# Performance work log

Hardware: AMD Instinct MI355X
Metric: run time of the kernel (lower is better)

The kernel has to match this reference:

```python
import math
import jax, jax.numpy as jnp
import numpy as np

D = 4  # BWGNN d


def calculate_theta2(d):
    # Faithful numeric reimplementation of the sympy version.
    # f_i(x) = (x/2)^i (1-x/2)^(d-i) / (2*Beta(i+1, d+1-i)); the original code
    # keeps only the d lowest-order (ascending) coefficients, dropping x^d.
    thetas = []
    for i in range(d):
        c1 = np.zeros(i + 1); c1[i] = 0.5 ** i                      # (x/2)^i
        c2 = np.array([math.comb(d - i, j) * (-0.5) ** j
                       for j in range(d - i + 1)])                   # (1-x/2)^(d-i)
        c = np.convolve(c1, c2)                                      # ascending, len d+1
        B = math.factorial(i) * math.factorial(d - i) / math.factorial(d + 1)
        c = c / (2.0 * B)
        thetas.append([float(c[j]) for j in range(d)])               # coeff[d-i] slicing
    return thetas

THETAS = calculate_theta2(D)


def setup_inputs() -> dict:
    key = jax.random.key(0)
    k1, k2, k3, k4 = jax.random.split(key, 4)
    N, E, F_in, H = 100000, 1600000, 128, 64
    feature = jax.random.normal(k1, (N, F_in), dtype=jnp.float32)
    edge_index = jax.random.randint(k2, (2, E), 0, N, dtype=jnp.int32)
    W = jax.random.normal(k3, (F_in, H), dtype=jnp.float32) * 0.05
    b = jax.random.normal(k4, (H,), dtype=jnp.float32) * 0.05
    return {"feature": feature, "edge_index": edge_index, "W": W, "b": b}


def reference(feature, edge_index, W, b):
    N = feature.shape[0]
    src, dst = edge_index[0], edge_index[1]
    # out_degrees: number of out-edges per node (src side), clamped to >= 1
    deg = jax.ops.segment_sum(jnp.ones_like(src, dtype=jnp.float32), src,
                              num_segments=N)
    D_invsqrt = jnp.maximum(deg, 1.0) ** -0.5  # [N]
    D_invsqrt = D_invsqrt[:, None]             # [N,1]

    h = jax.nn.leaky_relu(feature @ W + b, negative_slope=0.01)  # [N,H]

    def unn_laplacian(feat):
        # feat - D^{-1/2} A^T D^{-1/2} feat  (copy_u + sum over dst)
        msg = (feat * D_invsqrt)[src]                          # [E,H]
        agg = jax.ops.segment_sum(msg, dst, num_segments=N)    # [N,H]
        return feat - agg * D_invsqrt

    outs = []
    for theta in THETAS:
        feat = h
        acc = theta[0] * feat
        for k in range(1, len(theta)):
            feat = unn_laplacian(feat)
            acc = acc + theta[k] * feat
        outs.append(acc)
    return jnp.concatenate(outs, axis=1)  # [N, len(THETAS)*H]
```

## Files before the change

### kernel.cpp

```cpp
#include <hip/hip_runtime.h>

#define THREADS 256
#define T1 4096
#define BCAP 8192
#define NBMAX 512

__device__ __forceinline__ float bf2f(unsigned short u) {
    return __uint_as_float(((unsigned int)u) << 16);
}
__device__ __forceinline__ unsigned short f2bf(float x) {
    unsigned int u = __float_as_uint(x);
    u += 0x7fffu + ((u >> 16) & 1u);
    return (unsigned short)(u >> 16);
}
__device__ __forceinline__ float blo(unsigned int x) { return __uint_as_float(x << 16); }
__device__ __forceinline__ float bhi(unsigned int x) { return __uint_as_float(x & 0xffff0000u); }

__global__ void zero_kernel(int* __restrict__ p, int n) {
    const int i = blockIdx.x * blockDim.x + threadIdx.x;
    if (i < n) p[i] = 0;
}

__global__ void bin_kernel(const int* __restrict__ src, const int* __restrict__ dst,
                           int* __restrict__ gFillD, unsigned int* __restrict__ gBufD,
                           int* __restrict__ gFillS, unsigned int* __restrict__ gBufS,
                           int E, int tiles) {
    __shared__ int cnt[NBMAX], scanB[NBMAX], gbase[NBMAX], place[NBMAX];
    __shared__ unsigned int stage[T1], addr[T1];
    const int tid = threadIdx.x;
    const bool isS = blockIdx.x >= tiles;
    const int tile = isS ? blockIdx.x - tiles : blockIdx.x;
    const int* key = isS ? src : dst;
    int* gFill = isS ? gFillS : gFillD;
    unsigned int* gBuf = isS ? gBufS : gBufD;
    const int tileStart = tile * T1;
    const int tileCnt = min(T1, E - tileStart);

    for (int i = tid; i < NBMAX; i += THREADS) { cnt[i] = 0; place[i] = 0; }
    __syncthreads();

    for (int i = tid; i < tileCnt; i += THREADS)
        atomicAdd(&cnt[key[tileStart + i] >> 8], 1);
    __syncthreads();

    if (tid < 64) {
        const int base = tid * 8;
        int loc[8]; int s = 0;
        #pragma unroll
        for (int k = 0; k < 8; ++k) { loc[k] = s; s += cnt[base + k]; }
        int run = s;
        #pragma unroll
        for (int off = 1; off < 64; off <<= 1) {
            int t = __shfl_up(run, off);
            if (tid >= off) run += t;
        }
        const int excl = run - s;
        #pragma unroll
        for (int k = 0; k < 8; ++k) scanB[base + k] = excl + loc[k];
    }
    __syncthreads();

    for (int i = tid; i < NBMAX; i += THREADS)
        gbase[i] = atomicAdd(&gFill[i], cnt[i]);
    __syncthreads();

    for (int i = tid; i < tileCnt; i += THREADS) {
        const int kk = key[tileStart + i];
        const int b = kk >> 8;
        const unsigned int rec = isS ? (unsigned int)(kk & 255)
                                     : (((unsigned int)(kk & 255) << 17) | (unsigned int)src[tileStart + i]);
        const int pos = atomicAdd(&place[b], 1);
        const int li = scanB[b] + pos;
        const int gi = gbase[b] + pos;
        stage[li] = rec;
        addr[li] = (gi < BCAP) ? (unsigned int)(b * BCAP + gi) : 0xFFFFFFFFu;
    }
    __syncthreads();

    for (int i = tid; i < tileCnt; i += THREADS) {
        const unsigned int a = addr[i];
        if (a != 0xFFFFFFFFu) gBuf[a] = stage[i];
    }
}

__global__ void scanb_kernel(const int* __restrict__ gFill, int* __restrict__ gBase,
                             int* __restrict__ rowptr, int nb, int N) {
    __shared__ int s[NBMAX];
    const int tid = threadIdx.x;
    const int v = (tid < nb) ? min(gFill[tid], BCAP) : 0;
    s[tid] = v;
    __syncthreads();
    for (int off = 1; off < NBMAX; off <<= 1) {
        int t = (tid >= off) ? s[tid - off] : 0;
        __syncthreads();
        s[tid] += t;
        __syncthreads();
    }
    if (tid < nb) gBase[tid] = s[tid] - v;
    if (tid == NBMAX - 1) rowptr[N] = s[NBMAX - 1];
}

__global__ void csr_kernel(const int* __restrict__ gFillD, const int* __restrict__ gBase,
                           const unsigned int* __restrict__ gBufD,
                           const int* __restrict__ gFillS, const unsigned int* __restrict__ gBufS,
                           int* __restrict__ rowptr, int* __restrict__ col,
                           int* __restrict__ deg, int N) {
    __shared__ int fillT[256], offT[256], place[256], sc[256];
    __shared__ int colT[BCAP];
    __shared__ int nwrite;
    const int tid = threadIdx.x;
    const int b = blockIdx.x;
    const int nrec = min(gFillD[b], BCAP);
    const int base = gBase[b];

    fillT[tid] = 0; place[tid] = 0;
    __syncthreads();
    for (int i = tid; i < nrec; i += THREADS)
        atomicAdd(&fillT[gBufD[(size_t)b * BCAP + i] >> 17], 1);
    __syncthreads();

    int v = fillT[tid];
    sc[tid] = v;
    __syncthreads();
    for (int off = 1; off < 256; off <<= 1) {
        int t = (tid >= off) ? sc[tid - off] : 0;
        __syncthreads();
        sc[tid] += t;
        __syncthreads();
    }
    offT[tid] = sc[tid] - v;
    if (tid == 255) nwrite = sc[255];
    __syncthreads();

    const int node0 = b << 8;
    const int nvalid = min(256, N - node0);
    if (tid < nvalid) rowptr[node0 + tid] = base + offT[tid];

    for (int i = tid; i < nrec; i += THREADS) {
        const unsigned int rec = gBufD[(size_t)b * BCAP + i];
        const int dlow = rec >> 17;
        const int s = rec & 0x1FFFF;
        const int pos = atomicAdd(&place[dlow], 1);
        colT[offT[dlow] + pos] = s;
    }
    __syncthreads();

    const int nw = nwrite;
    for (int i = tid; i < nw; i += THREADS) col[base + i] = colT[i];

    fillT[tid] = 0;
    __syncthreads();
    const int nrecS = min(gFillS[b], BCAP);
    for (int i = tid; i < nrecS; i += THREADS)
        atomicAdd(&fillT[gBufS[(size_t)b * BCAP + i] & 255], 1);
    __syncthreads();
    if (tid < nvalid) deg[node0 + tid] = fillT[tid];
}

__global__ void count_fb(const int* __restrict__ src, const int* __restrict__ dst,
                         int* __restrict__ deg, int* __restrict__ cntd, int E) {
    const int stride = gridDim.x * blockDim.x;
    for (int i = blockIdx.x * blockDim.x + threadIdx.x; i < E; i += stride) {
        atomicAdd(&deg[src[i]], 1);
        atomicAdd(&cntd[dst[i]], 1);
    }
}
__global__ void scan_fb(const int* __restrict__ cnt, int* __restrict__ rowptr, int N) {
    __shared__ int s[256];
    __shared__ int carry;
    const int tid = threadIdx.x;
    if (tid == 0) carry = 0;
    __syncthreads();
    for (int basei = 0; basei < N; basei += 256) {
        const int i = basei + tid;
        const int v = (i < N) ? cnt[i] : 0;
        s[tid] = v;
        __syncthreads();
        for (int off = 1; off < 256; off <<= 1) {
            int t = (tid >= off) ? s[tid - off] : 0;
            __syncthreads();
            s[tid] += t;
            __syncthreads();
        }
        if (i < N) rowptr[i] = carry + s[tid] - v;
        __syncthreads();
        if (tid == 0) carry += s[255];
        __syncthreads();
    }
    if (tid == 0) rowptr[N] = carry;
}
__global__ void fill_fb(const int* __restrict__ src, const int* __restrict__ dst,
                        const int* __restrict__ rowptr, int* __restrict__ place,
                        int* __restrict__ col, int E) {
    const int stride = gridDim.x * blockDim.x;
    for (int i = blockIdx.x * blockDim.x + threadIdx.x; i < E; i += stride) {
        const int d = dst[i];
        col[rowptr[d] + atomicAdd(&place[d], 1)] = src[i];
    }
}

__global__ void gemm_leaky(const float* __restrict__ feat, const float* __restrict__ W,
                           const float* __restrict__ b, const int* __restrict__ deg,
                           unsigned short* __restrict__ S0, int N) {
    __shared__ float Wl[128 * 64];
    __shared__ float fl_t[128][65];
    __shared__ float bl[64];

    {
        const float4* W4 = (const float4*)W;
        float4* Wl4 = (float4*)Wl;
        for (int i = threadIdx.x; i < 2048; i += THREADS) Wl4[i] = W4[i];
        if (threadIdx.x < 64) bl[threadIdx.x] = b[threadIdx.x];
    }

    const int cg = threadIdx.x & 15;
    const int rg = threadIdx.x >> 4;
    const int ntiles = (N + 63) >> 6;

    for (int tile = blockIdx.x; tile < ntiles; tile += gridDim.x) {
        const int n0 = tile << 6;
        __syncthreads();
        for (int i = threadIdx.x; i < 2048; i += THREADS) {
            const int rr = i >> 5;
            const int kk = i & 31;
            float4 v = make_float4(0.f, 0.f, 0.f, 0.f);
            if (n0 + rr < N) v = ((const float4*)(feat + (size_t)(n0 + rr) * 128))[kk];
            fl_t[kk * 4 + 0][rr] = v.x;
            fl_t[kk * 4 + 1][rr] = v.y;
            fl_t[kk * 4 + 2][rr] = v.z;
            fl_t[kk * 4 + 3][rr] = v.w;
        }
        __syncthreads();

        float acc[4][4];
        #pragma unroll
        for (int j = 0; j < 4; ++j) {
            float bv = bl[cg * 4 + j];
            acc[0][j] = bv; acc[1][j] = bv; acc[2][j] = bv; acc[3][j] = bv;
        }

        #pragma unroll 4
        for (int k = 0; k < 128; ++k) {
            const float4 w = *((const float4*)&Wl[k * 64 + cg * 4]);
            const float4 f = *((const float4*)&fl_t[k][rg * 4]);
            acc[0][0] += f.x * w.x; acc[0][1] += f.x * w.y; acc[0][2] += f.x * w.z; acc[0][3] += f.x * w.w;
            acc[1][0] += f.y * w.x; acc[1][1] += f.y * w.y; acc[1][2] += f.y * w.z; acc[1][3] += f.y * w.w;
            acc[2][0] += f.z * w.x; acc[2][1] += f.z * w.y; acc[2][2] += f.z * w.z; acc[2][3] += f.z * w.w;
            acc[3][0] += f.w * w.x; acc[3][1] += f.w * w.y; acc[3][2] += f.w * w.z; acc[3][3] += f.w * w.w;
        }

        #pragma unroll
        for (int i = 0; i < 4; ++i) {
            const int n = n0 + rg * 4 + i;
            if (n < N) {
                const float dv = rsqrtf(fmaxf((float)deg[n], 1.0f));
                ushort4 o;
                float v0 = acc[i][0] > 0.f ? acc[i][0] : 0.01f * acc[i][0];
                float v1 = acc[i][1] > 0.f ? acc[i][1] : 0.01f * acc[i][1];
                float v2 = acc[i][2] > 0.f ? acc[i][2] : 0.01f * acc[i][2];
                float v3 = acc[i][3] > 0.f ? acc[i][3] : 0.01f * acc[i][3];
                o.x = f2bf(v0 * dv); o.y = f2bf(v1 * dv); o.z = f2bf(v2 * dv); o.w = f2bf(v3 * dv);
                *((ushort4*)(S0 + (size_t)n * 64 + cg * 4)) = o;
            }
        }
    }
}

template<bool FINAL>
__global__ void hop_kernel(const int* __restrict__ rowptr, const int* __restrict__ col,
                           const int* __restrict__ deg,
                           const unsigned short* __restrict__ Sprev,
                           unsigned short* __restrict__ Snext,
                           const unsigned short* __restrict__ S0,
                           const unsigned short* __restrict__ S1,
                           float* __restrict__ out, int N) {
    const int lane = threadIdx.x & 63;
    const int g = lane >> 3;
    const int q = lane & 7;
    const int nwaves = (gridDim.x * blockDim.x) >> 6;
    for (int n = (blockIdx.x * blockDim.x + threadIdx.x) >> 6; n < N; n += nwaves) {
        const int beg = rowptr[n];
        const int end = rowptr[n + 1];
        float a[8];
        #pragma unroll
        for (int k = 0; k < 8; ++k) a[k] = 0.f;

        for (int e0 = beg; e0 < end; e0 += 64) {
            const int idx = e0 + lane;
            const int c = (idx < end) ? col[idx] : 0;
            const int m = min(64, end - e0);
            for (int j = 0; j < m; j += 16) {
                const int jg0 = j + g;
                const int jg1 = j + 8 + g;
                const int s0 = __shfl(c, jg0 & 63);
                const int s1 = __shfl(c, jg1 & 63);
                const bool v0 = jg0 < m;
                const bool v1 = jg1 < m;
                uint4 u0, u1;
                if (v0) u0 = *(const uint4*)(Sprev + (size_t)s0 * 64 + q * 8);
                if (v1) u1 = *(const uint4*)(Sprev + (size_t)s1 * 64 + q * 8);
                if (v0) {
                    a[0] += blo(u0.x); a[1] += bhi(u0.x);
                    a[2] += blo(u0.y); a[3] += bhi(u0.y);
                    a[4] += blo(u0.z); a[5] += bhi(u0.z);
                    a[6] += blo(u0.w); a[7] += bhi(u0.w);
                }
                if (v1) {
                    a[0] += blo(u1.x); a[1] += bhi(u1.x);
                    a[2] += blo(u1.y); a[3] += bhi(u1.y);
                    a[4] += blo(u1.z); a[5] += bhi(u1.z);
                    a[6] += blo(u1.w); a[7] += bhi(u1.w);
                }
            }
        }
        #pragma unroll
        for (int k = 0; k < 8; ++k) {
            a[k] += __shfl_xor(a[k], 8);
            a[k] += __shfl_xor(a[k], 16);
            a[k] += __shfl_xor(a[k], 32);
        }

        const float d = fmaxf((float)deg[n], 1.0f);
        const float inv = 1.0f / d;
        const uint4 uo = *(const uint4*)(Sprev + (size_t)n * 64 + q * 8);
        float own[8], sn[8];
        own[0] = blo(uo.x); own[1] = bhi(uo.x); own[2] = blo(uo.y); own[3] = bhi(uo.y);
        own[4] = blo(uo.z); own[5] = bhi(uo.z); own[6] = blo(uo.w); own[7] = bhi(uo.w);
        #pragma unroll
        for (int k = 0; k < 8; ++k) sn[k] = own[k] - a[k] * inv;

        if (!FINAL) {
            if (g == 0) {
                uint4 w;
                w.x = (unsigned int)f2bf(sn[0]) | ((unsigned int)f2bf(sn[1]) << 16);
                w.y = (unsigned int)f2bf(sn[2]) | ((unsigned int)f2bf(sn[3]) << 16);
                w.z = (unsigned int)f2bf(sn[4]) | ((unsigned int)f2bf(sn[5]) << 16);
                w.w = (unsigned int)f2bf(sn[6]) | ((unsigned int)f2bf(sn[7]) << 16);
                *((uint4*)(Snext + (size_t)n * 64 + q * 8)) = w;
            }
        } else if (g < 4) {
            const float sc = sqrtf(d);
            const uint4 u0 = *(const uint4*)(S0 + (size_t)n * 64 + q * 8);
            const uint4 u1 = *(const uint4*)(S1 + (size_t)n * 64 + q * 8);
            float h[8], p1[8];
            h[0] = blo(u0.x); h[1] = bhi(u0.x); h[2] = blo(u0.y); h[3] = bhi(u0.y);
            h[4] = blo(u0.z); h[5] = bhi(u0.z); h[6] = blo(u0.w); h[7] = bhi(u0.w);
            p1[0] = blo(u1.x); p1[1] = bhi(u1.x); p1[2] = blo(u1.y); p1[3] = bhi(u1.y);
            p1[4] = blo(u1.z); p1[5] = bhi(u1.z); p1[6] = blo(u1.w); p1[7] = bhi(u1.w);
            float c0, c1, c2, c3;
            if (g == 0)      { c0 = 2.5f; c1 = -5.0f; c2 = 3.75f;  c3 = -1.25f; }
            else if (g == 1) { c0 = 0.f;  c1 = 5.0f;  c2 = -7.5f;  c3 = 3.75f;  }
            else if (g == 2) { c0 = 0.f;  c1 = 0.f;   c2 = 3.75f;  c3 = -3.75f; }
            else             { c0 = 0.f;  c1 = 0.f;   c2 = 0.f;    c3 = 1.25f;  }
            float o[8];
            #pragma unroll
            for (int k = 0; k < 8; ++k) {
                const float hv = h[k] * sc, p1v = p1[k] * sc, p2v = own[k] * sc, p3v = sn[k] * sc;
                o[k] = c0 * hv + c1 * p1v + c2 * p2v + c3 * p3v;
            }
            float* op = out + (size_t)n * 256 + g * 64 + q * 8;
            *((float4*)op)       = make_float4(o[0], o[1], o[2], o[3]);
            *((float4*)(op + 4)) = make_float4(o[4], o[5], o[6], o[7]);
        }
    }
}

extern "C" void kernel_launch(void* const* d_in, const int* in_sizes, int n_in,
                              void* d_out, int out_size, void* d_ws, size_t ws_size,
                              hipStream_t stream) {
    const float* feature = (const float*)d_in[0];
    const int*   eidx    = (const int*)d_in[1];
    const float* W       = (const float*)d_in[2];
    const float* b       = (const float*)d_in[3];
    float* out = (float*)d_out;

    const int N = in_sizes[0] / 128;
    const int E = in_sizes[1] / 2;
    const int* src = eidx;
    const int* dst = eidx + E;

    const int nb = (N + 255) >> 8;

    int* deg    = (int*)d_ws;
    int* fill   = deg + N;
    int* rowptr = fill + N;
    int* col    = rowptr + (N + 1);
    int* gFillD = col + E;
    int* gFillS = gFillD + NBMAX;
    int* gBase  = gFillS + NBMAX;
    unsigned int* gBufD = (unsigned int*)(gBase + NBMAX);
    unsigned int* gBufS = gBufD + (size_t)nb * BCAP;
    unsigned short* S0 = (unsigned short*)(((uintptr_t)(gBufS + (size_t)nb * BCAP) + 255) & ~(uintptr_t)255);
    unsigned short* S1 = S0 + (size_t)N * 64;
    unsigned short* S2 = S1 + (size_t)N * 64;

    if (N <= 131072) {
        zero_kernel<<<(2 * NBMAX + THREADS - 1) / THREADS, THREADS, 0, stream>>>(gFillD, 2 * NBMAX);
        const int tiles = (E + T1 - 1) / T1;
        bin_kernel<<<2 * tiles, THREADS, 0, stream>>>(src, dst, gFillD, gBufD, gFillS, gBufS, E, tiles);
        scanb_kernel<<<1, NBMAX, 0, stream>>>(gFillD, gBase, rowptr, nb, N);
        csr_kernel<<<nb, THREADS, 0, stream>>>(gFillD, gBase, gBufD, gFillS, gBufS, rowptr, col, deg, N);
    } else {
        zero_kernel<<<(2 * N + THREADS - 1) / THREADS, THREADS, 0, stream>>>(deg, 2 * N);
        count_fb<<<2048, THREADS, 0, stream>>>(src, dst, deg, fill, E);
        scan_fb<<<1, 256, 0, stream>>>(fill, rowptr, N);
        zero_kernel<<<(N + THREADS - 1) / THREADS, THREADS, 0, stream>>>(fill, N);
        fill_fb<<<2048, THREADS, 0, stream>>>(src, dst, rowptr, fill, col, E);
    }

    const int gemm_blocks = (N + 63) / 64;
    gemm_leaky<<<gemm_blocks, THREADS, 0, stream>>>(feature, W, b, deg, S0, N);

    const int gblocks = (N + 3) / 4;
    hop_kernel<false><<<gblocks, THREADS, 0, stream>>>(rowptr, col, deg, S0, S1, S0, S0, out, N);
    hop_kernel<false><<<gblocks, THREADS, 0, stream>>>(rowptr, col, deg, S1, S2, S0, S0, out, N);
    hop_kernel<true ><<<gblocks, THREADS, 0, stream>>>(rowptr, col, deg, S2, S2, S0, S1, out, N);
}
```

Baseline: 234.2 us.

## Fuse bucket scan into CSR build, shrink source records, nontemporal output stores

Removes the separate single-block scan kernel by having each CSR block recompute the bucket prefix sum itself, which saves one launch and its serialization. Source-side bin records become single bytes instead of 32-bit words, cutting the traffic for degree counting. The bin kernel now loads its keys into registers once and reuses them for counting and placement, and the final output is written with nontemporal stores. The cost is redundant scan work in every CSR block and extra register pressure in the bin kernel.

```diff
diff --git a/kernel.cpp b/kernel.cpp
--- a/kernel.cpp
+++ b/kernel.cpp
@@ -5,6 +5,8 @@
 #define BCAP 8192
 #define NBMAX 512
 
+typedef float nfloat4 __attribute__((ext_vector_type(4)));
+
 __device__ __forceinline__ float bf2f(unsigned short u) {
     return __uint_as_float(((unsigned int)u) << 16);
 }
@@ -23,24 +25,37 @@
 
 __global__ void bin_kernel(const int* __restrict__ src, const int* __restrict__ dst,
                            int* __restrict__ gFillD, unsigned int* __restrict__ gBufD,
-                           int* __restrict__ gFillS, unsigned int* __restrict__ gBufS,
+                           int* __restrict__ gFillS, unsigned char* __restrict__ gBufS,
                            int E, int tiles) {
     __shared__ int cnt[NBMAX], scanB[NBMAX], gbase[NBMAX], place[NBMAX];
-    __shared__ unsigned int stage[T1], addr[T1];
+    __shared__ unsigned int stage[T1];
+    __shared__ unsigned int addr[T1];
     const int tid = threadIdx.x;
     const bool isS = blockIdx.x >= tiles;
     const int tile = isS ? blockIdx.x - tiles : blockIdx.x;
     const int* key = isS ? src : dst;
     int* gFill = isS ? gFillS : gFillD;
-    unsigned int* gBuf = isS ? gBufS : gBufD;
     const int tileStart = tile * T1;
     const int tileCnt = min(T1, E - tileStart);
 
+    int kv[16], pv[16];
+    #pragma unroll
+    for (int it = 0; it < 16; ++it) {
+        const int i = tid + it * THREADS;
+        if (i < tileCnt) {
+            kv[it] = key[tileStart + i];
+            if (!isS) pv[it] = src[tileStart + i];
+        }
+    }
+
     for (int i = tid; i < NBMAX; i += THREADS) { cnt[i] = 0; place[i] = 0; }
     __syncthreads();
 
-    for (int i = tid; i < tileCnt; i += THREADS)
-        atomicAdd(&cnt[key[tileStart + i] >> 8], 1);
+    #pragma unroll
+    for (int it = 0; it < 16; ++it) {
+        const int i = tid + it * THREADS;
+        if (i < tileCnt) atomicAdd(&cnt[kv[it] >> 8], 1);
+    }
     __syncthreads();
 
     if (tid < 64) {
@@ -64,54 +79,69 @@
         gbase[i] = atomicAdd(&gFill[i], cnt[i]);
     __syncthreads();
 
-    for (int i = tid; i < tileCnt; i += THREADS) {
-        const int kk = key[tileStart + i];
-        const int b = kk >> 8;
-        const unsigned int rec = isS ? (unsigned int)(kk & 255)
-                                     : (((unsigned int)(kk & 255) << 17) | (unsigned int)src[tileStart + i]);
-        const int pos = atomicAdd(&place[b], 1);
-        const int li = scanB[b] + pos;
-        const int gi = gbase[b] + pos;
-        stage[li] = rec;
-        addr[li] = (gi < BCAP) ? (unsigned int)(b * BCAP + gi) : 0xFFFFFFFFu;
-    }
-    __syncthreads();
-
-    for (int i = tid; i < tileCnt; i += THREADS) {
-        const unsigned int a = addr[i];
-        if (a != 0xFFFFFFFFu) gBuf[a] = stage[i];
-    }
-}
-
-__global__ void scanb_kernel(const int* __restrict__ gFill, int* __restrict__ gBase,
-                             int* __restrict__ rowptr, int nb, int N) {
-    __shared__ int s[NBMAX];
-    const int tid = threadIdx.x;
-    const int v = (tid < nb) ? min(gFill[tid], BCAP) : 0;
-    s[tid] = v;
-    __syncthreads();
-    for (int off = 1; off < NBMAX; off <<= 1) {
-        int t = (tid >= off) ? s[tid - off] : 0;
-        __syncthreads();
-        s[tid] += t;
-        __syncthreads();
-    }
-    if (tid < nb) gBase[tid] = s[tid] - v;
-    if (tid == NBMAX - 1) rowptr[N] = s[NBMAX - 1];
-}
-
-__global__ void csr_kernel(const int* __restrict__ gFillD, const int* __restrict__ gBase,
-                           const unsigned int* __restrict__ gBufD,
-                           const int* __restrict__ gFillS, const unsigned int* __restrict__ gBufS,
+    unsigned char* stageB = (unsigned char*)stage;
+    #pragma unroll
+    for (int it = 0; it < 16; ++it) {
+        const int i = tid + it * THREADS;
+        if (i < tileCnt) {
+            const int kk = kv[it];
+            const int b = kk >> 8;
+            const int pos = atomicAdd(&place[b], 1);
+            const int li = scanB[b] + pos;
+            const int gi = gbase[b] + pos;
+            if (isS) stageB[li] = (unsigned char)(kk & 255);
+            else     stage[li] = ((unsigned int)(kk & 255) << 17) | (unsigned int)pv[it];
+            addr[li] = (gi < BCAP) ? (unsigned int)(b * BCAP + gi) : 0xFFFFFFFFu;
+        }
+    }
+    __syncthreads();
+
+    if (isS) {
+        for (int i = tid; i < tileCnt; i += THREADS) {
+            const unsigned int a = addr[i];
+            if (a != 0xFFFFFFFFu) gBufS[a] = stageB[i];
+        }
+    } else {
+        for (int i = tid; i < tileCnt; i += THREADS) {
+            const unsigned int a = addr[i];
+            if (a != 0xFFFFFFFFu) gBufD[a] = stage[i];
+        }
+    }
+}
+
+__global__ void csr_kernel(const int* __restrict__ gFillD, const unsigned int* __restrict__ gBufD,
+                           const int* __restrict__ gFillS, const unsigned char* __restrict__ gBufS,
                            int* __restrict__ rowptr, int* __restrict__ col,
-                           int* __restrict__ deg, int N) {
+                           int* __restrict__ deg, int N, int nb) {
+    __shared__ int sg[NBMAX], scanG[NBMAX];
     __shared__ int fillT[256], offT[256], place[256], sc[256];
     __shared__ int colT[BCAP];
     __shared__ int nwrite;
     const int tid = threadIdx.x;
     const int b = blockIdx.x;
-    const int nrec = min(gFillD[b], BCAP);
-    const int base = gBase[b];
+
+    for (int i = tid; i < NBMAX; i += THREADS) sg[i] = (i < nb) ? min(gFillD[i], BCAP) : 0;
+    __syncthreads();
+    if (tid < 64) {
+        const int base = tid * 8;
+        int loc[8]; int s = 0;
+        #pragma unroll
+        for (int k = 0; k < 8; ++k) { loc[k] = s; s += sg[base + k]; }
+        int run = s;
+        #pragma unroll
+        for (int off = 1; off < 64; off <<= 1) {
+            int t = __shfl_up(run, off);
+            if (tid >= off) run += t;
+        }
+        const int excl = run - s;
+        #pragma unroll
+        for (int k = 0; k < 8; ++k) scanG[base + k] = excl + loc[k];
+    }
+    __syncthreads();
+
+    const int nrec = sg[b];
+    const int base = scanG[b];
+    if (b == 0 && tid == 0) rowptr[N] = scanG[NBMAX - 1] + sg[NBMAX - 1];
 
     fillT[tid] = 0; place[tid] = 0;
     __syncthreads();
@@ -152,7 +182,7 @@
     __syncthreads();
     const int nrecS = min(gFillS[b], BCAP);
     for (int i = tid; i < nrecS; i += THREADS)
-        atomicAdd(&fillT[gBufS[(size_t)b * BCAP + i] & 255], 1);
+        atomicAdd(&fillT[gBufS[(size_t)b * BCAP + i]], 1);
     __syncthreads();
     if (tid < nvalid) deg[node0 + tid] = fillT[tid];
 }
@@ -359,8 +389,10 @@
                 o[k] = c0 * hv + c1 * p1v + c2 * p2v + c3 * p3v;
             }
             float* op = out + (size_t)n * 256 + g * 64 + q * 8;
-            *((float4*)op)       = make_float4(o[0], o[1], o[2], o[3]);
-            *((float4*)(op + 4)) = make_float4(o[4], o[5], o[6], o[7]);
+            nfloat4 w0 = { o[0], o[1], o[2], o[3] };
+            nfloat4 w1 = { o[4], o[5], o[6], o[7] };
+            __builtin_nontemporal_store(w0, (nfloat4*)op);
+            __builtin_nontemporal_store(w1, (nfloat4*)(op + 4));
         }
     }
 }
@@ -387,9 +419,8 @@
     int* col    = rowptr + (N + 1);
     int* gFillD = col + E;
     int* gFillS = gFillD + NBMAX;
-    int* gBase  = gFillS + NBMAX;
-    unsigned int* gBufD = (unsigned int*)(gBase + NBMAX);
-    unsigned int* gBufS = gBufD + (size_t)nb * BCAP;
+    unsigned int* gBufD = (unsigned int*)(gFillS + NBMAX);
+    unsigned char* gBufS = (unsigned char*)(gBufD + (size_t)nb * BCAP);
     unsigned short* S0 = (unsigned short*)(((uintptr_t)(gBufS + (size_t)nb * BCAP) + 255) & ~(uintptr_t)255);
     unsigned short* S1 = S0 + (size_t)N * 64;
     unsigned short* S2 = S1 + (size_t)N * 64;
@@ -398,8 +429,7 @@
         zero_kernel<<<(2 * NBMAX + THREADS - 1) / THREADS, THREADS, 0, stream>>>(gFillD, 2 * NBMAX);
         const int tiles = (E + T1 - 1) / T1;
         bin_kernel<<<2 * tiles, THREADS, 0, stream>>>(src, dst, gFillD, gBufD, gFillS, gBufS, E, tiles);
-        scanb_kernel<<<1, NBMAX, 0, stream>>>(gFillD, gBase, rowptr, nb, N);
-        csr_kernel<<<nb, THREADS, 0, stream>>>(gFillD, gBase, gBufD, gFillS, gBufS, rowptr, col, deg, N);
+        csr_kernel<<<nb, THREADS, 0, stream>>>(gFillD, gBufD, gFillS, gBufS, rowptr, col, deg, N, nb);
     } else {
         zero_kernel<<<(2 * N + THREADS - 1) / THREADS, THREADS, 0, stream>>>(deg, 2 * N);
         count_fb<<<2048, THREADS, 0, stream>>>(src, dst, deg, fill, E);
```

Measured after the change: 232.2 us, median of 2. About the same (-0.9%).
